# Kernel optimization log

Hardware: AMD Instinct MI355X
Metric: run time of the kernel (lower is better)

The kernel has to match this reference:

```python
import jax, jax.numpy as jnp
import numpy as np

NUM_EXPERTS = 8
VOCAB_SIZE = 100000
H = 1024
IE = 512  # intermediate_size // num_experts
B, S = 4, 8192


def setup_inputs() -> dict:
    key = jax.random.key(0)
    ks = jax.random.split(key, 8)
    return {
        "hidden_states": jax.random.normal(ks[0], (B, S, H), dtype=jnp.float32),
        "token_ids": jax.random.randint(ks[1], (B, S), 0, VOCAB_SIZE, dtype=jnp.int64),
        "gate_w": jax.random.normal(ks[2], (NUM_EXPERTS, H, IE), dtype=jnp.float32) * 0.02,
        "up_w": jax.random.normal(ks[3], (NUM_EXPERTS, H, IE), dtype=jnp.float32) * 0.02,
        "down_w": jax.random.normal(ks[4], (NUM_EXPERTS, IE, H), dtype=jnp.float32) * 0.02,
        "shared_gate_w": jax.random.normal(ks[5], (IE, H), dtype=jnp.float32) * 0.02,
        "shared_up_w": jax.random.normal(ks[6], (IE, H), dtype=jnp.float32) * 0.02,
        "shared_down_w": jax.random.normal(ks[7], (H, IE), dtype=jnp.float32) * 0.02,
    }


def reference(hidden_states, token_ids, gate_w, up_w, down_w,
              shared_gate_w, shared_up_w, shared_down_w):
    Bq, Sq, Hq = hidden_states.shape
    flat_x = hidden_states.reshape(-1, Hq)                    # [N, H]
    ids = jnp.clip(token_ids, 0, VOCAB_SIZE - 1).reshape(-1)  # [N]
    # token_to_expert buffer is arange(V) % E (no token_frequencies given)
    expert_ids = ids % NUM_EXPERTS                            # [N]

    # shared dense SwiGLU expert (torch Linear: x @ W.T)
    shared_out = (jax.nn.silu(flat_x @ shared_gate_w.T)
                  * (flat_x @ shared_up_w.T)) @ shared_down_w.T

    # routed experts: loop over the small fixed expert set, mask-combine
    routed_out = jnp.zeros_like(flat_x)
    for e in range(NUM_EXPERTS):
        mask = (expert_ids == e)[:, None]                     # [N, 1]
        inter = jax.nn.silu(flat_x @ gate_w[e]) * (flat_x @ up_w[e])  # [N, IE]
        routed_out = routed_out + jnp.where(mask, inter @ down_w[e], 0.0)

    return (routed_out + shared_out).reshape(Bq, Sq, Hq)
```

## Files before the change

### kernel.cpp

```cpp
#include <hip/hip_runtime.h>
#include <hip/hip_bf16.h>


#define N_TOK 32768
#define HD 1024
#define NE 8

typedef __attribute__((ext_vector_type(8))) short bf16x8;
typedef __attribute__((ext_vector_type(8))) unsigned short u16x8;
typedef __attribute__((ext_vector_type(4))) float f32x4;

__device__ __forceinline__ unsigned short f2bf(float f) {
  unsigned int x = __float_as_uint(f);
  x += 0x7fffu + ((x >> 16) & 1u);
  return (unsigned short)(x >> 16);
}

__device__ __forceinline__ void gld16(const unsigned short* g, unsigned short* l) {
  __builtin_amdgcn_global_load_lds(
      (const __attribute__((address_space(1))) unsigned int*)g,
      (__attribute__((address_space(3))) unsigned int*)l,
      16, 0, 0);
}

__device__ __forceinline__ int expert_of(int id) {
  int v = id < 0 ? 0 : (id > 99999 ? 99999 : id);
  return v & 7;
}

__global__ void k_zero(int* ctrl) {
  if (threadIdx.x < 16) ctrl[threadIdx.x] = 0;
}

__global__ void k_count(const int* __restrict__ ids, int* __restrict__ cnt) {
  __shared__ int l[NE];
  if (threadIdx.x < NE) l[threadIdx.x] = 0;
  __syncthreads();
  int t = blockIdx.x * 256 + threadIdx.x;
  atomicAdd(&l[expert_of(ids[t])], 1);
  __syncthreads();
  if (threadIdx.x < NE) atomicAdd(&cnt[threadIdx.x], l[threadIdx.x]);
}

__global__ void k_scan(const int* __restrict__ cnt, int* __restrict__ off) {
  if (threadIdx.x == 0 && blockIdx.x == 0) {
    int a = 0;
    for (int e = 0; e < NE; e++) { off[e] = a; a += (cnt[e] + 127) & ~127; }
    off[NE] = a;
  }
}

__global__ void k_fill(const int* __restrict__ ids, int* __restrict__ cursor,
                       const int* __restrict__ off, int* __restrict__ perm) {
  __shared__ int lcnt[NE], lbase[NE];
  if (threadIdx.x < NE) lcnt[threadIdx.x] = 0;
  __syncthreads();
  int t = blockIdx.x * 256 + threadIdx.x;
  int e = expert_of(ids[t]);
  int r = atomicAdd(&lcnt[e], 1);
  __syncthreads();
  if (threadIdx.x < NE)
    lbase[threadIdx.x] = atomicAdd(&cursor[threadIdx.x], lcnt[threadIdx.x]);
  __syncthreads();
  perm[off[e] + lbase[e] + r] = t;
}

__global__ void k_cvt_x(const float* __restrict__ src, unsigned short* __restrict__ dst) {
  size_t i = ((size_t)blockIdx.x * 256 + threadIdx.x) * 8;
  float4 a = *reinterpret_cast<const float4*>(src + i);
  float4 b = *reinterpret_cast<const float4*>(src + i + 4);
  u16x8 o;
  o[0]=f2bf(a.x); o[1]=f2bf(a.y); o[2]=f2bf(a.z); o[3]=f2bf(a.w);
  o[4]=f2bf(b.x); o[5]=f2bf(b.y); o[6]=f2bf(b.z); o[7]=f2bf(b.w);
  *reinterpret_cast<u16x8*>(dst + i) = o;
}

__device__ __forceinline__ int rowmap(int c, int mode) {
  if (mode == 0) return c;
  return ((c >> 4) << 5) + (c & 15) + (mode == 2 ? 16 : 0);
}

__global__ void k_transpose_cvt(const float* __restrict__ src0, unsigned short* __restrict__ dst0,
                                int C, int mode, size_t src_estride, size_t dst_estride) {
  const float* src = src0 + blockIdx.z * src_estride;
  unsigned short* dst = dst0 + blockIdx.z * dst_estride;
  __shared__ __attribute__((aligned(16))) float tile[32][33];
  int t = threadIdx.x;
  int r0 = blockIdx.y * 32, c0 = blockIdx.x * 32;
  int row = t >> 3, c4 = (t & 7) * 4;
  float4 v = *reinterpret_cast<const float4*>(src + (size_t)(r0 + row) * C + c0 + c4);
  tile[row][c4+0] = v.x; tile[row][c4+1] = v.y; tile[row][c4+2] = v.z; tile[row][c4+3] = v.w;
  __syncthreads();
  ushort4 o;
  o.x = f2bf(tile[c4+0][row]); o.y = f2bf(tile[c4+1][row]);
  o.z = f2bf(tile[c4+2][row]); o.w = f2bf(tile[c4+3][row]);
  int orow = rowmap(c0 + row, mode);
  *reinterpret_cast<ushort4*>(dst + (size_t)orow * HD + r0 + c4) = o;
}

__global__ void k_copy_cvt(const float* __restrict__ src, unsigned short* __restrict__ dst,
                           int cols, int mode, int dcol, size_t dst_estride) {
  size_t i = ((size_t)blockIdx.x * 256 + threadIdx.x) * 4;
  int r = (int)(i / cols), c = (int)(i % cols);
  int row = (mode == 0) ? r : (1024 + rowmap(r, mode));
  float4 v = *reinterpret_cast<const float4*>(src + i);
  ushort4 o; o.x=f2bf(v.x); o.y=f2bf(v.y); o.z=f2bf(v.z); o.w=f2bf(v.w);
  *reinterpret_cast<ushort4*>(dst + blockIdx.z * dst_estride
                              + (size_t)row * HD + dcol + c) = o;
}

__global__ __launch_bounds__(512, 2) void k_gu(
    const unsigned short* __restrict__ xbf,
    const unsigned short* __restrict__ W1,
    const int* __restrict__ perm, const int* __restrict__ cnt, const int* __restrict__ off,
    unsigned short* __restrict__ inter) {
  const int e = blockIdx.z;
  const int ce = cnt[e];
  const int m0 = blockIdx.y * 256;
  if (m0 >= ce) return;
  const int cep = (ce + 127) & ~127;
  const int n0 = blockIdx.x * 256;
  const int oe = off[e];
  __shared__ __attribute__((aligned(16))) unsigned short sm[65536];
  const int tid = threadIdx.x;
  const int lane = tid & 63;
  const int wv = tid >> 6;
  const int wm = wv >> 2, wn = wv & 3;

  const int r0s = ((tid >> 6) << 4) | (tid & 15);
  const int r1s = r0s + 128;
  const int kb = ((tid >> 4) & 3) * 8;
  int ia = m0 + r0s; if (ia > ce - 1) ia = ce - 1;
  int ib = m0 + r1s; if (ib > ce - 1) ib = ce - 1;
  const unsigned short* gA0 = xbf + (size_t)perm[oe + ia] * HD + kb;
  const unsigned short* gA1 = xbf + (size_t)perm[oe + ib] * HD + kb;
  const unsigned short* gB0 = W1 + ((size_t)e << 21) + (size_t)(n0 + r0s) * HD + kb;
  const unsigned short* gB1 = W1 + ((size_t)e << 21) + (size_t)(n0 + r1s) * HD + kb;

  f32x4 acc[8][4];
#pragma unroll
  for (int mi = 0; mi < 8; mi++)
#pragma unroll
    for (int ni = 0; ni < 4; ni++) acc[mi][ni] = (f32x4){0.f, 0.f, 0.f, 0.f};

  auto STAGE = [&](int b, int kt) {
    const int ko = kt * 32;
    unsigned short* la = sm + b * 8192 + wv * 512;
    unsigned short* lb = sm + 32768 + b * 8192 + wv * 512;
    gld16(gA0 + ko, la);
    gld16(gA1 + ko, la + 4096);
    gld16(gB0 + ko, lb);
    gld16(gB1 + ko, lb + 4096);
  };
  auto COMPUTE = [&](int b) {
    const unsigned short* A = sm + b * 8192;
    const unsigned short* B = sm + 32768 + b * 8192;
    bf16x8 a[8], bb[4];
#pragma unroll
    for (int mi = 0; mi < 8; mi++)
      a[mi] = *reinterpret_cast<const bf16x8*>(A + (wm * 8 + mi) * 512 + lane * 8);
#pragma unroll
    for (int ni = 0; ni < 4; ni++)
      bb[ni] = *reinterpret_cast<const bf16x8*>(B + (wn * 4 + ni) * 512 + lane * 8);
    __builtin_amdgcn_s_setprio(1);
#pragma unroll
    for (int mi = 0; mi < 8; mi++)
#pragma unroll
      for (int ni = 0; ni < 4; ni++)
        acc[mi][ni] = __builtin_amdgcn_mfma_f32_16x16x32_bf16(a[mi], bb[ni], acc[mi][ni], 0, 0, 0);
    __builtin_amdgcn_s_setprio(0);
  };

  STAGE(0, 0); STAGE(1, 1); STAGE(2, 2);
#pragma unroll 1
  for (int kt = 0; kt < 29; kt++) {
    STAGE((kt + 3) & 3, kt + 3);
    asm volatile("s_waitcnt vmcnt(12)\n\ts_barrier" ::: "memory");
    COMPUTE(kt & 3);
    asm volatile("s_barrier" ::: "memory");
  }
  asm volatile("s_waitcnt vmcnt(8)\n\ts_barrier" ::: "memory");
  COMPUTE(1);
  asm volatile("s_barrier" ::: "memory");
  asm volatile("s_waitcnt vmcnt(4)\n\ts_barrier" ::: "memory");
  COMPUTE(2);
  asm volatile("s_barrier" ::: "memory");
  asm volatile("s_waitcnt vmcnt(0)\n\ts_barrier" ::: "memory");
  COMPUTE(3);

  const int colbase = (n0 + wn * 64) >> 1;
#pragma unroll
  for (int mi = 0; mi < 8; mi++)
#pragma unroll
    for (int p = 0; p < 2; p++)
#pragma unroll
      for (int r = 0; r < 4; r++) {
        int m = wm * 128 + mi * 16 + (lane >> 4) * 4 + r;
        if (m0 + m < cep) {
          float g = acc[mi][2 * p][r];
          float u = acc[mi][2 * p + 1][r];
          float sv = g / (1.f + __expf(-g)) * u;
          inter[(size_t)(oe + m0 + m) * HD + colbase + p * 16 + (lane & 15)] = f2bf(sv);
        }
      }
}

__global__ __launch_bounds__(512, 2) void k_down(
    const unsigned short* __restrict__ inter,
    const unsigned short* __restrict__ Dt,
    const int* __restrict__ perm, const int* __restrict__ cnt, const int* __restrict__ off,
    float* __restrict__ out) {
  const int e = blockIdx.z;
  const int ce = cnt[e];
  const int m0 = blockIdx.y * 256;
  if (m0 >= ce) return;
  const int cep = (ce + 127) & ~127;
  const int n0 = blockIdx.x * 256;
  const int oe = off[e];
  __shared__ __attribute__((aligned(16))) unsigned short sm[65536];
  const int tid = threadIdx.x;
  const int lane = tid & 63;
  const int wv = tid >> 6;
  const int wm = wv >> 2, wn = wv & 3;

  const int r0s = ((tid >> 6) << 4) | (tid & 15);
  const int r1s = r0s + 128;
  const int kb = ((tid >> 4) & 3) * 8;
  int ia = m0 + r0s; if (ia > cep - 1) ia = cep - 1;
  int ib = m0 + r1s; if (ib > cep - 1) ib = cep - 1;
  const unsigned short* gA0 = inter + (size_t)(oe + ia) * HD + kb;
  const unsigned short* gA1 = inter + (size_t)(oe + ib) * HD + kb;
  const unsigned short* gB0 = Dt + ((size_t)e << 20) + (size_t)(n0 + r0s) * HD + kb;
  const unsigned short* gB1 = Dt + ((size_t)e << 20) + (size_t)(n0 + r1s) * HD + kb;

  f32x4 acc[8][4];
#pragma unroll
  for (int mi = 0; mi < 8; mi++)
#pragma unroll
    for (int ni = 0; ni < 4; ni++) acc[mi][ni] = (f32x4){0.f, 0.f, 0.f, 0.f};

  auto STAGE = [&](int b, int kt) {
    const int ko = kt * 32;
    unsigned short* la = sm + b * 8192 + wv * 512;
    unsigned short* lb = sm + 32768 + b * 8192 + wv * 512;
    gld16(gA0 + ko, la);
    gld16(gA1 + ko, la + 4096);
    gld16(gB0 + ko, lb);
    gld16(gB1 + ko, lb + 4096);
  };
  auto COMPUTE = [&](int b) {
    const unsigned short* A = sm + b * 8192;
    const unsigned short* B = sm + 32768 + b * 8192;
    bf16x8 a[8], bb[4];
#pragma unroll
    for (int mi = 0; mi < 8; mi++)
      a[mi] = *reinterpret_cast<const bf16x8*>(A + (wm * 8 + mi) * 512 + lane * 8);
#pragma unroll
    for (int ni = 0; ni < 4; ni++)
      bb[ni] = *reinterpret_cast<const bf16x8*>(B + (wn * 4 + ni) * 512 + lane * 8);
    __builtin_amdgcn_s_setprio(1);
#pragma unroll
    for (int mi = 0; mi < 8; mi++)
#pragma unroll
      for (int ni = 0; ni < 4; ni++)
        acc[mi][ni] = __builtin_amdgcn_mfma_f32_16x16x32_bf16(a[mi], bb[ni], acc[mi][ni], 0, 0, 0);
    __builtin_amdgcn_s_setprio(0);
  };

  STAGE(0, 0); STAGE(1, 1); STAGE(2, 2);
#pragma unroll 1
  for (int kt = 0; kt < 29; kt++) {
    STAGE((kt + 3) & 3, kt + 3);
    asm volatile("s_waitcnt vmcnt(12)\n\ts_barrier" ::: "memory");
    COMPUTE(kt & 3);
    asm volatile("s_barrier" ::: "memory");
  }
  asm volatile("s_waitcnt vmcnt(8)\n\ts_barrier" ::: "memory");
  COMPUTE(1);
  asm volatile("s_barrier" ::: "memory");
  asm volatile("s_waitcnt vmcnt(4)\n\ts_barrier" ::: "memory");
  COMPUTE(2);
  asm volatile("s_barrier" ::: "memory");
  asm volatile("s_waitcnt vmcnt(0)\n\ts_barrier" ::: "memory");
  COMPUTE(3);

#pragma unroll
  for (int mi = 0; mi < 8; mi++)
#pragma unroll
    for (int r = 0; r < 4; r++) {
      int m = wm * 128 + mi * 16 + (lane >> 4) * 4 + r;
      int gm = m0 + m;
      if (gm < ce) {
        int t = perm[oe + gm];
#pragma unroll
        for (int ni = 0; ni < 4; ni++)
          out[(size_t)t * HD + n0 + wn * 64 + ni * 16 + (lane & 15)] = acc[mi][ni][r];
      }
    }
}

__global__ __launch_bounds__(256) void k_naive(
    const float* __restrict__ x, const int* __restrict__ ids,
    const float* __restrict__ gw, const float* __restrict__ uw, const float* __restrict__ dw,
    const float* __restrict__ sgw, const float* __restrict__ suw, const float* __restrict__ sdw,
    float* __restrict__ out) {
  const int t = blockIdx.x;
  const int tid = threadIdx.x;
  __shared__ float sx[1024];
  __shared__ float si[1024];
  for (int i = tid; i < 1024; i += 256) sx[i] = x[(size_t)t * 1024 + i];
  const int e = expert_of(ids[t]);
  __syncthreads();
  const float* gwe = gw + (size_t)e * 1024 * 512;
  const float* uwe = uw + (size_t)e * 1024 * 512;
  for (int j = tid; j < 512; j += 256) {
    float g = 0, u = 0, sg = 0, su = 0;
    for (int k = 0; k < 1024; k++) {
      float xv = sx[k];
      g += xv * gwe[(size_t)k * 512 + j];
      u += xv * uwe[(size_t)k * 512 + j];
      sg += xv * sgw[(size_t)j * 1024 + k];
      su += xv * suw[(size_t)j * 1024 + k];
    }
    si[j] = g / (1.f + __expf(-g)) * u;
    si[512 + j] = sg / (1.f + __expf(-sg)) * su;
  }
  __syncthreads();
  const float* dwe = dw + (size_t)e * 512 * 1024;
  for (int n = tid; n < 1024; n += 256) {
    float a = 0;
    for (int k = 0; k < 512; k++)
      a += si[k] * dwe[(size_t)k * 1024 + n] + si[512 + k] * sdw[(size_t)n * 512 + k];
    out[(size_t)t * 1024 + n] = a;
  }
}

extern "C" void kernel_launch(void* const* d_in, const int* in_sizes, int n_in,
                              void* d_out, int out_size, void* d_ws, size_t ws_size,
                              hipStream_t stream) {
  const float* x = (const float*)d_in[0];
  const int* ids = (const int*)d_in[1];
  const float* gw = (const float*)d_in[2];
  const float* uw = (const float*)d_in[3];
  const float* dw = (const float*)d_in[4];
  const float* sgw = (const float*)d_in[5];
  const float* suw = (const float*)d_in[6];
  const float* sdw = (const float*)d_in[7];
  float* out = (float*)d_out;

  const size_t REQ = 186908672ull;
  if (ws_size < REQ) {
    k_naive<<<N_TOK, 256, 0, stream>>>(x, ids, gw, uw, dw, sgw, suw, sdw, out);
    return;
  }

  char* ws = (char*)d_ws;
  int* ctrl = (int*)ws;
  int* perm = (int*)(ws + 1024);
  unsigned short* xbf = (unsigned short*)(ws + 262144);
  unsigned short* W1 = (unsigned short*)(ws + 67371008ull);
  unsigned short* Dt = (unsigned short*)(ws + 100925440ull);
  unsigned short* inter = (unsigned short*)(ws + 117702656ull);

  k_zero<<<1, 64, 0, stream>>>(ctrl);
  k_count<<<128, 256, 0, stream>>>(ids, ctrl);
  k_scan<<<1, 64, 0, stream>>>(ctrl, ctrl + 16);
  k_fill<<<128, 256, 0, stream>>>(ids, ctrl + 8, ctrl + 16, perm);
  k_cvt_x<<<16384, 256, 0, stream>>>(x, xbf);
  k_transpose_cvt<<<dim3(16, 32, 8), 256, 0, stream>>>(gw, W1, 512, 1,
                                                       (size_t)1024 * 512, (size_t)1 << 21);
  k_transpose_cvt<<<dim3(16, 32, 8), 256, 0, stream>>>(uw, W1, 512, 2,
                                                       (size_t)1024 * 512, (size_t)1 << 21);
  k_transpose_cvt<<<dim3(32, 16, 8), 256, 0, stream>>>(dw, Dt, 1024, 0,
                                                       (size_t)512 * 1024, (size_t)1 << 20);
  k_copy_cvt<<<dim3(512, 1, 8), 256, 0, stream>>>(sgw, W1, 1024, 1, 0, (size_t)1 << 21);
  k_copy_cvt<<<dim3(512, 1, 8), 256, 0, stream>>>(suw, W1, 1024, 2, 0, (size_t)1 << 21);
  k_copy_cvt<<<dim3(512, 1, 8), 256, 0, stream>>>(sdw, Dt, 512, 0, 512, (size_t)1 << 20);
  k_gu<<<dim3(8, 128, 8), 512, 0, stream>>>(xbf, W1, perm, ctrl, ctrl + 16, inter);
  k_down<<<dim3(4, 128, 8), 512, 0, stream>>>(inter, Dt, perm, ctrl, ctrl + 16, out);
}
```

Before: 415.6 us.

## Restructure GEMM mainloop into finer-grained interleaved load/compute phases

Both grouped GEMM kernels replace the 4-stage K=32 ring buffer with a 2-buffer K=64 scheme. Each K-tile is split into half-K, half-M phases, and individual A and B global-to-LDS loads are interleaved between the phases. The intent is to spread memory issue more evenly across MFMA work and to cut register pressure by loading only 4 A fragments at a time. The cost is more barriers per K-step and a shallower prefetch depth, which could expose load latency.

```diff
diff --git a/kernel.cpp b/kernel.cpp
--- a/kernel.cpp
+++ b/kernel.cpp
@@ -127,15 +127,14 @@
   const int wv = tid >> 6;
   const int wm = wv >> 2, wn = wv & 3;
 
-  const int r0s = ((tid >> 6) << 4) | (tid & 15);
-  const int r1s = r0s + 128;
-  const int kb = ((tid >> 4) & 3) * 8;
-  int ia = m0 + r0s; if (ia > ce - 1) ia = ce - 1;
-  int ib = m0 + r1s; if (ib > ce - 1) ib = ce - 1;
-  const unsigned short* gA0 = xbf + (size_t)perm[oe + ia] * HD + kb;
-  const unsigned short* gA1 = xbf + (size_t)perm[oe + ib] * HD + kb;
-  const unsigned short* gB0 = W1 + ((size_t)e << 21) + (size_t)(n0 + r0s) * HD + kb;
-  const unsigned short* gB1 = W1 + ((size_t)e << 21) + (size_t)(n0 + r1s) * HD + kb;
+  const int srow = wv * 16 + (tid & 15);
+  const int srck = ((tid >> 4) & 3) * 8;
+  int ia = m0 + srow;        if (ia > ce - 1) ia = ce - 1;
+  int ib = m0 + 128 + srow;  if (ib > ce - 1) ib = ce - 1;
+  const unsigned short* pA0 = xbf + (size_t)perm[oe + ia] * HD + srck;
+  const unsigned short* pA1 = xbf + (size_t)perm[oe + ib] * HD + srck;
+  const unsigned short* pB0 = W1 + ((size_t)e << 21) + (size_t)(n0 + srow) * HD + srck;
+  const unsigned short* pB1 = W1 + ((size_t)e << 21) + (size_t)(n0 + 128 + srow) * HD + srck;
 
   f32x4 acc[8][4];
 #pragma unroll
@@ -143,50 +142,65 @@
 #pragma unroll
     for (int ni = 0; ni < 4; ni++) acc[mi][ni] = (f32x4){0.f, 0.f, 0.f, 0.f};
 
-  auto STAGE = [&](int b, int kt) {
-    const int ko = kt * 32;
-    unsigned short* la = sm + b * 8192 + wv * 512;
-    unsigned short* lb = sm + 32768 + b * 8192 + wv * 512;
-    gld16(gA0 + ko, la);
-    gld16(gA1 + ko, la + 4096);
-    gld16(gB0 + ko, lb);
-    gld16(gB1 + ko, lb + 4096);
-  };
-  auto COMPUTE = [&](int b) {
-    const unsigned short* A = sm + b * 8192;
-    const unsigned short* B = sm + 32768 + b * 8192;
-    bf16x8 a[8], bb[4];
-#pragma unroll
-    for (int mi = 0; mi < 8; mi++)
-      a[mi] = *reinterpret_cast<const bf16x8*>(A + (wm * 8 + mi) * 512 + lane * 8);
-#pragma unroll
-    for (int ni = 0; ni < 4; ni++)
-      bb[ni] = *reinterpret_cast<const bf16x8*>(B + (wn * 4 + ni) * 512 + lane * 8);
+  auto stageA = [&](int b, int ks, int kt) {
+    unsigned short* d = sm + b * 16384 + ks * 8192 + wv * 512;
+    const int ko = kt * 64 + ks * 32;
+    gld16(pA0 + ko, d);
+    gld16(pA1 + ko, d + 4096);
+  };
+  auto stageB = [&](int b, int ks, int kt) {
+    unsigned short* d = sm + 32768 + b * 16384 + ks * 8192 + wv * 512;
+    const int ko = kt * 64 + ks * 32;
+    gld16(pB0 + ko, d);
+    gld16(pB1 + ko, d + 4096);
+  };
+
+  bf16x8 bb[4];
+  auto phase = [&](int b, int ks, int mh) {
+    asm volatile("s_barrier" ::: "memory");
+    const unsigned short* Ar = sm + b * 16384 + ks * 8192;
+    if (mh == 0) {
+      const unsigned short* Br = sm + 32768 + b * 16384 + ks * 8192;
+#pragma unroll
+      for (int ni = 0; ni < 4; ni++)
+        bb[ni] = *reinterpret_cast<const bf16x8*>(Br + (wn * 4 + ni) * 512 + lane * 8);
+    }
+    bf16x8 a[4];
+#pragma unroll
+    for (int j = 0; j < 4; j++)
+      a[j] = *reinterpret_cast<const bf16x8*>(Ar + (wm * 8 + mh * 4 + j) * 512 + lane * 8);
     __builtin_amdgcn_s_setprio(1);
 #pragma unroll
-    for (int mi = 0; mi < 8; mi++)
+    for (int j = 0; j < 4; j++)
 #pragma unroll
       for (int ni = 0; ni < 4; ni++)
-        acc[mi][ni] = __builtin_amdgcn_mfma_f32_16x16x32_bf16(a[mi], bb[ni], acc[mi][ni], 0, 0, 0);
+        acc[mh * 4 + j][ni] = __builtin_amdgcn_mfma_f32_16x16x32_bf16(a[j], bb[ni], acc[mh * 4 + j][ni], 0, 0, 0);
     __builtin_amdgcn_s_setprio(0);
-  };
-
-  STAGE(0, 0); STAGE(1, 1); STAGE(2, 2);
+    asm volatile("s_barrier" ::: "memory");
+  };
+
+  stageA(0, 0, 0); stageB(0, 0, 0); stageA(0, 1, 0); stageB(0, 1, 0);
+  stageA(1, 0, 1); stageB(1, 0, 1);
 #pragma unroll 1
-  for (int kt = 0; kt < 29; kt++) {
-    STAGE((kt + 3) & 3, kt + 3);
-    asm volatile("s_waitcnt vmcnt(12)\n\ts_barrier" ::: "memory");
-    COMPUTE(kt & 3);
-    asm volatile("s_barrier" ::: "memory");
-  }
-  asm volatile("s_waitcnt vmcnt(8)\n\ts_barrier" ::: "memory");
-  COMPUTE(1);
-  asm volatile("s_barrier" ::: "memory");
-  asm volatile("s_waitcnt vmcnt(4)\n\ts_barrier" ::: "memory");
-  COMPUTE(2);
-  asm volatile("s_barrier" ::: "memory");
-  asm volatile("s_waitcnt vmcnt(0)\n\ts_barrier" ::: "memory");
-  COMPUTE(3);
+  for (int j = 0; j < 7; j++) {
+    const int t1 = 2 * j + 1, t2 = 2 * j + 2, t3 = 2 * j + 3;
+    stageA(1, 1, t1); asm volatile("s_waitcnt vmcnt(10)" ::: "memory"); phase(0, 0, 0);
+    stageB(1, 1, t1);                                                   phase(0, 0, 1);
+    stageA(0, 0, t2); asm volatile("s_waitcnt vmcnt(10)" ::: "memory"); phase(0, 1, 0);
+    stageB(0, 0, t2);                                                   phase(0, 1, 1);
+    stageA(0, 1, t2); asm volatile("s_waitcnt vmcnt(10)" ::: "memory"); phase(1, 0, 0);
+    stageB(0, 1, t2);                                                   phase(1, 0, 1);
+    stageA(1, 0, t3); asm volatile("s_waitcnt vmcnt(10)" ::: "memory"); phase(1, 1, 0);
+    stageB(1, 0, t3);                                                   phase(1, 1, 1);
+  }
+  stageA(1, 1, 15); asm volatile("s_waitcnt vmcnt(10)" ::: "memory"); phase(0, 0, 0);
+  stageB(1, 1, 15);                                                   phase(0, 0, 1);
+  asm volatile("s_waitcnt vmcnt(8)" ::: "memory");                    phase(0, 1, 0);
+                                                                      phase(0, 1, 1);
+  asm volatile("s_waitcnt vmcnt(4)" ::: "memory");                    phase(1, 0, 0);
+                                                                      phase(1, 0, 1);
+  asm volatile("s_waitcnt vmcnt(0)" ::: "memory");                    phase(1, 1, 0);
+                                                                      phase(1, 1, 1);
 
   const int colbase = (n0 + wn * 64) >> 1;
 #pragma unroll
@@ -223,15 +237,14 @@
   const int wv = tid >> 6;
   const int wm = wv >> 2, wn = wv & 3;
 
-  const int r0s = ((tid >> 6) << 4) | (tid & 15);
-  const int r1s = r0s + 128;
-  const int kb = ((tid >> 4) & 3) * 8;
-  int ia = m0 + r0s; if (ia > cep - 1) ia = cep - 1;
-  int ib = m0 + r1s; if (ib > cep - 1) ib = cep - 1;
-  const unsigned short* gA0 = inter + (size_t)(oe + ia) * HD + kb;
-  const unsigned short* gA1 = inter + (size_t)(oe + ib) * HD + kb;
-  const unsigned short* gB0 = Dt + ((size_t)e << 20) + (size_t)(n0 + r0s) * HD + kb;
-  const unsigned short* gB1 = Dt + ((size_t)e << 20) + (size_t)(n0 + r1s) * HD + kb;
+  const int srow = wv * 16 + (tid & 15);
+  const int srck = ((tid >> 4) & 3) * 8;
+  int ia = m0 + srow;        if (ia > cep - 1) ia = cep - 1;
+  int ib = m0 + 128 + srow;  if (ib > cep - 1) ib = cep - 1;
+  const unsigned short* pA0 = inter + (size_t)(oe + ia) * HD + srck;
+  const unsigned short* pA1 = inter + (size_t)(oe + ib) * HD + srck;
+  const unsigned short* pB0 = Dt + ((size_t)e << 20) + (size_t)(n0 + srow) * HD + srck;
+  const unsigned short* pB1 = Dt + ((size_t)e << 20) + (size_t)(n0 + 128 + srow) * HD + srck;
 
   f32x4 acc[8][4];
 #pragma unroll
@@ -239,50 +252,65 @@
 #pragma unroll
     for (int ni = 0; ni < 4; ni++) acc[mi][ni] = (f32x4){0.f, 0.f, 0.f, 0.f};
 
-  auto STAGE = [&](int b, int kt) {
-    const int ko = kt * 32;
-    unsigned short* la = sm + b * 8192 + wv * 512;
-    unsigned short* lb = sm + 32768 + b * 8192 + wv * 512;
-    gld16(gA0 + ko, la);
-    gld16(gA1 + ko, la + 4096);
-    gld16(gB0 + ko, lb);
-    gld16(gB1 + ko, lb + 4096);
-  };
-  auto COMPUTE = [&](int b) {
-    const unsigned short* A = sm + b * 8192;
-    const unsigned short* B = sm + 32768 + b * 8192;
-    bf16x8 a[8], bb[4];
-#pragma unroll
-    for (int mi = 0; mi < 8; mi++)
-      a[mi] = *reinterpret_cast<const bf16x8*>(A + (wm * 8 + mi) * 512 + lane * 8);
-#pragma unroll
-    for (int ni = 0; ni < 4; ni++)
-      bb[ni] = *reinterpret_cast<const bf16x8*>(B + (wn * 4 + ni) * 512 + lane * 8);
+  auto stageA = [&](int b, int ks, int kt) {
+    unsigned short* d = sm + b * 16384 + ks * 8192 + wv * 512;
+    const int ko = kt * 64 + ks * 32;
+    gld16(pA0 + ko, d);
+    gld16(pA1 + ko, d + 4096);
+  };
+  auto stageB = [&](int b, int ks, int kt) {
+    unsigned short* d = sm + 32768 + b * 16384 + ks * 8192 + wv * 512;
+    const int ko = kt * 64 + ks * 32;
+    gld16(pB0 + ko, d);
+    gld16(pB1 + ko, d + 4096);
+  };
+
+  bf16x8 bb[4];
+  auto phase = [&](int b, int ks, int mh) {
+    asm volatile("s_barrier" ::: "memory");
+    const unsigned short* Ar = sm + b * 16384 + ks * 8192;
+    if (mh == 0) {
+      const unsigned short* Br = sm + 32768 + b * 16384 + ks * 8192;
+#pragma unroll
+      for (int ni = 0; ni < 4; ni++)
+        bb[ni] = *reinterpret_cast<const bf16x8*>(Br + (wn * 4 + ni) * 512 + lane * 8);
+    }
+    bf16x8 a[4];
+#pragma unroll
+    for (int j = 0; j < 4; j++)
+      a[j] = *reinterpret_cast<const bf16x8*>(Ar + (wm * 8 + mh * 4 + j) * 512 + lane * 8);
     __builtin_amdgcn_s_setprio(1);
 #pragma unroll
-    for (int mi = 0; mi < 8; mi++)
+    for (int j = 0; j < 4; j++)
 #pragma unroll
       for (int ni = 0; ni < 4; ni++)
-        acc[mi][ni] = __builtin_amdgcn_mfma_f32_16x16x32_bf16(a[mi], bb[ni], acc[mi][ni], 0, 0, 0);
+        acc[mh * 4 + j][ni] = __builtin_amdgcn_mfma_f32_16x16x32_bf16(a[j], bb[ni], acc[mh * 4 + j][ni], 0, 0, 0);
     __builtin_amdgcn_s_setprio(0);
-  };
-
-  STAGE(0, 0); STAGE(1, 1); STAGE(2, 2);
+    asm volatile("s_barrier" ::: "memory");
+  };
+
+  stageA(0, 0, 0); stageB(0, 0, 0); stageA(0, 1, 0); stageB(0, 1, 0);
+  stageA(1, 0, 1); stageB(1, 0, 1);
 #pragma unroll 1
-  for (int kt = 0; kt < 29; kt++) {
-    STAGE((kt + 3) & 3, kt + 3);
-    asm volatile("s_waitcnt vmcnt(12)\n\ts_barrier" ::: "memory");
-    COMPUTE(kt & 3);
-    asm volatile("s_barrier" ::: "memory");
-  }
-  asm volatile("s_waitcnt vmcnt(8)\n\ts_barrier" ::: "memory");
-  COMPUTE(1);
-  asm volatile("s_barrier" ::: "memory");
-  asm volatile("s_waitcnt vmcnt(4)\n\ts_barrier" ::: "memory");
-  COMPUTE(2);
-  asm volatile("s_barrier" ::: "memory");
-  asm volatile("s_waitcnt vmcnt(0)\n\ts_barrier" ::: "memory");
-  COMPUTE(3);
+  for (int j = 0; j < 7; j++) {
+    const int t1 = 2 * j + 1, t2 = 2 * j + 2, t3 = 2 * j + 3;
+    stageA(1, 1, t1); asm volatile("s_waitcnt vmcnt(10)" ::: "memory"); phase(0, 0, 0);
+    stageB(1, 1, t1);                                                   phase(0, 0, 1);
+    stageA(0, 0, t2); asm volatile("s_waitcnt vmcnt(10)" ::: "memory"); phase(0, 1, 0);
+    stageB(0, 0, t2);                                                   phase(0, 1, 1);
+    stageA(0, 1, t2); asm volatile("s_waitcnt vmcnt(10)" ::: "memory"); phase(1, 0, 0);
+    stageB(0, 1, t2);                                                   phase(1, 0, 1);
+    stageA(1, 0, t3); asm volatile("s_waitcnt vmcnt(10)" ::: "memory"); phase(1, 1, 0);
+    stageB(1, 0, t3);                                                   phase(1, 1, 1);
+  }
+  stageA(1, 1, 15); asm volatile("s_waitcnt vmcnt(10)" ::: "memory"); phase(0, 0, 0);
+  stageB(1, 1, 15);                                                   phase(0, 0, 1);
+  asm volatile("s_waitcnt vmcnt(8)" ::: "memory");                    phase(0, 1, 0);
+                                                                      phase(0, 1, 1);
+  asm volatile("s_waitcnt vmcnt(4)" ::: "memory");                    phase(1, 0, 0);
+                                                                      phase(1, 0, 1);
+  asm volatile("s_waitcnt vmcnt(0)" ::: "memory");                    phase(1, 1, 0);
+                                                                      phase(1, 1, 1);
 
 #pragma unroll
   for (int mi = 0; mi < 8; mi++)
```

Result: faster. 396.2 us (-4.7%).
